# Performance work log

Hardware: AMD Instinct MI355X
Metric: run time of the kernel (lower is better)

Reference implementation:

```python
import jax, jax.numpy as jnp
import numpy as np

INPUT, HIDDEN, LAYERS, OUT = 512, 512, 2, 512
B, T = 128, 1024


def _gru_cell(x, h, w_ih, w_hh, b_ih, b_hh):
    # x: [B, D_in], h: [B, H]; w_ih: [3H, D_in], w_hh: [3H, H]
    gi = x @ w_ih.T + b_ih
    gh = h @ w_hh.T + b_hh
    i_r, i_z, i_n = jnp.split(gi, 3, axis=-1)
    h_r, h_z, h_n = jnp.split(gh, 3, axis=-1)
    r = jax.nn.sigmoid(i_r + h_r)
    z = jax.nn.sigmoid(i_z + h_z)
    n = jnp.tanh(i_n + r * h_n)
    return (1.0 - z) * n + z * h


def setup_inputs() -> dict:
    key = jax.random.key(0)
    ks = jax.random.split(key, 11)
    s = 1.0 / np.sqrt(HIDDEN)
    u = lambda k, shp: jax.random.uniform(k, shp, jnp.float32, -s, s)
    return {
        "x": jax.random.normal(ks[0], (B, T, INPUT), jnp.float32),
        "w_ih0": u(ks[1], (3 * HIDDEN, INPUT)),
        "w_hh0": u(ks[2], (3 * HIDDEN, HIDDEN)),
        "b_ih0": u(ks[3], (3 * HIDDEN,)),
        "b_hh0": u(ks[4], (3 * HIDDEN,)),
        "w_ih1": u(ks[5], (3 * HIDDEN, HIDDEN)),
        "w_hh1": u(ks[6], (3 * HIDDEN, HIDDEN)),
        "b_ih1": u(ks[7], (3 * HIDDEN,)),
        "b_hh1": u(ks[8], (3 * HIDDEN,)),
        "fc_w": u(ks[9], (OUT, HIDDEN)),
        "fc_b": u(ks[10], (OUT,)),
    }


def reference(x, w_ih0, w_hh0, b_ih0, b_hh0, w_ih1, w_hh1, b_ih1, b_hh1, fc_w, fc_b):
    xs = jnp.swapaxes(x, 0, 1)  # [T, B, INPUT]
    h0 = jnp.zeros((x.shape[0], HIDDEN), x.dtype)
    h1 = jnp.zeros((x.shape[0], HIDDEN), x.dtype)

    def step(carry, x_t):
        h0, h1 = carry
        h0 = _gru_cell(x_t, h0, w_ih0, w_hh0, b_ih0, b_hh0)
        h1 = _gru_cell(h0, h1, w_ih1, w_hh1, b_ih1, b_hh1)
        return (h0, h1), None

    (h0, h1), _ = jax.lax.scan(step, (h0, h1), xs)
    # final hidden of top layer -> fc (matches outs[-1].squeeze(); B>1 so squeeze is no-op)
    return h1 @ fc_w.T + fc_b
```

## Files before the change

kernel.cpp:

```cpp
#include <hip/hip_runtime.h>


#define TS   1024
#define HID  512
#define NWG  256
#define WGT  256

typedef __attribute__((ext_vector_type(8))) short bf16x8;
typedef __attribute__((ext_vector_type(4))) unsigned short u16x4;
typedef __attribute__((ext_vector_type(4))) float f32x4;

#define WS_FIN      2048
#define WS_HBUF     8192
#define HBUF_ELEMS  65536
#define WS_H1F      (WS_HBUF + 8 * HBUF_ELEMS * 2)
#define WS_ZERO     (WS_HBUF + 8 * HBUF_ELEMS * 2)

__device__ __forceinline__ unsigned short f2bf(float f) {
    unsigned u = __float_as_uint(f);
    u += 0x7FFFu + ((u >> 16) & 1u);
    return (unsigned short)(u >> 16);
}
__device__ __forceinline__ float bf2f(unsigned short s) {
    return __uint_as_float(((unsigned)s) << 16);
}
__device__ __forceinline__ float sigm(float v) { return 1.0f / (1.0f + __expf(-v)); }
__device__ __forceinline__ float tanh_(float v) { return 1.0f - 2.0f / (1.0f + __expf(2.0f * v)); }

__device__ __forceinline__ void st_agent8(void* p, unsigned long long v) {
    asm volatile("global_store_dwordx2 %0, %1, off sc1" :: "v"(p), "v"(v) : "memory");
}
__device__ __forceinline__ void st_agent16(void* p, f32x4 v) {
    asm volatile("global_store_dwordx4 %0, %1, off sc1" :: "v"(p), "v"(v) : "memory");
}
__device__ __forceinline__ void ld_agent16_issue(bf16x8& d, const unsigned short* p) {
    asm volatile("global_load_dwordx4 %0, %1, off sc1" : "=v"(d) : "v"(p));
}
__device__ __forceinline__ void ld16_issue(f32x4& d, const float* p) {
    asm volatile("global_load_dwordx4 %0, %1, off" : "=v"(d) : "v"(p));
}
__device__ __forceinline__ void wait_vm0() {
    asm volatile("s_waitcnt vmcnt(0)" ::: "memory");
    __builtin_amdgcn_sched_barrier(0);
}
__device__ __forceinline__ f32x4 ld_coh16f(const float* p) {
    const unsigned long long* q = (const unsigned long long*)p;
    union { unsigned long long u[2]; f32x4 v; } r;
    r.u[0] = __hip_atomic_load(q,     __ATOMIC_RELAXED, __HIP_MEMORY_SCOPE_AGENT);
    r.u[1] = __hip_atomic_load(q + 1, __ATOMIC_RELAXED, __HIP_MEMORY_SCOPE_AGENT);
    return r.v;
}

__global__ void __launch_bounds__(WGT, 1)
gru_persistent(const float* __restrict__ x,
               const float* __restrict__ wi0, const float* __restrict__ wh0,
               const float* __restrict__ bi0, const float* __restrict__ bh0,
               const float* __restrict__ wi1, const float* __restrict__ wh1,
               const float* __restrict__ bi1, const float* __restrict__ bh1,
               const float* __restrict__ fcw, const float* __restrict__ fcb,
               float* __restrict__ out, unsigned char* __restrict__ ws)
{
    __shared__ float ldsRed[3][64][49];

    const int tid   = threadIdx.x;
    const int lane  = tid & 63;
    const int kq    = tid >> 6;
    const int wgid  = blockIdx.x;
    const int layer = wgid >> 7;
    const int wid   = wgid & 127;
    const int mtile = wid & 7;
    const int ntile = wid >> 3;
    const int l15   = lane & 15;
    const int l4    = lane >> 4;
    const int gidx  = layer * 16 + ntile;

    unsigned* seqA = (unsigned*)(ws + (size_t)mtile * 256);
    unsigned* fin  = (unsigned*)(ws + WS_FIN);
    unsigned short* hbm = (unsigned short*)(ws + WS_HBUF);
    float* h1f = (float*)(ws + WS_H1F);

    unsigned short* h0hi[2] = { hbm + 0 * HBUF_ELEMS, hbm + 1 * HBUF_ELEMS };
    unsigned short* h0lo[2] = { hbm + 2 * HBUF_ELEMS, hbm + 3 * HBUF_ELEMS };
    unsigned short* h1hi[2] = { hbm + 4 * HBUF_ELEMS, hbm + 5 * HBUF_ELEMS };
    unsigned short* h1lo[2] = { hbm + 6 * HBUF_ELEMS, hbm + 7 * HBUF_ELEMS };

    bf16x8 wiR[4][6], whR[4][6];
    {
        const float* Wi = layer ? wi1 : wi0;
        const float* Wh = layer ? wh1 : wh0;
        #pragma unroll
        for (int kk = 0; kk < 4; ++kk) {
            const int kc = (kq << 2) + kk;
            #pragma unroll
            for (int f = 0; f < 6; ++f) {
                const int g = f >> 1, n2 = f & 1;
                const int jg = g * HID + ntile * 32 + n2 * 16 + l15;
                const float* pi = Wi + (size_t)jg * HID + kc * 32 + (l4 << 3);
                const float* ph = Wh + (size_t)jg * HID + kc * 32 + (l4 << 3);
                #pragma unroll
                for (int e = 0; e < 8; ++e) {
                    wiR[kk][f][e] = (short)f2bf(pi[e]);
                    whR[kk][f][e] = (short)f2bf(ph[e]);
                }
            }
        }
    }

    float br[2][4], bz[2][4], bni[2][4], bnh[2][4];
    if (kq == 0) {
        const float* Bi = layer ? bi1 : bi0;
        const float* Bh = layer ? bh1 : bh0;
        #pragma unroll
        for (int n2 = 0; n2 < 2; ++n2)
            #pragma unroll
            for (int r = 0; r < 4; ++r) {
                int j = ntile * 32 + n2 * 16 + (l4 << 2) + r;
                br[n2][r]  = Bi[j] + Bh[j];
                bz[n2][r]  = Bi[HID + j] + Bh[HID + j];
                bni[n2][r] = Bi[2 * HID + j];
                bnh[n2][r] = Bh[2 * HID + j];
            }
    } else {
        #pragma unroll
        for (int n2 = 0; n2 < 2; ++n2)
            #pragma unroll
            for (int r = 0; r < 4; ++r)
                br[n2][r] = bz[n2][r] = bni[n2][r] = bnh[n2][r] = 0.f;
    }

    float hold[2][4] = {{0,0,0,0},{0,0,0,0}};
    f32x4 acc_i[6], acc_h[6];
    #pragma unroll
    for (int f = 0; f < 6; ++f) {
        acc_i[f] = (f32x4){0.f,0.f,0.f,0.f};
        acc_h[f] = (f32x4){0.f,0.f,0.f,0.f};
    }

    f32x4 xs[4][2];

    auto splitPack = [](float a, float b, unsigned& hiw, unsigned& low) {
        unsigned ba = __float_as_uint(a), bb = __float_as_uint(b);
        unsigned ha = ba & 0xFFFF0000u,   hb = bb & 0xFFFF0000u;
        float la = a - __uint_as_float(ha);
        float lb = b - __uint_as_float(hb);
        hiw = (ba >> 16) | hb;
        low = (__float_as_uint(la) >> 16) | (__float_as_uint(lb) & 0xFFFF0000u);
    };

    auto do_window = [&]() {
        #pragma unroll
        for (int f = 0; f < 6; ++f) acc_i[f] = (f32x4){0.f,0.f,0.f,0.f};
        #pragma unroll
        for (int kk = 0; kk < 4; ++kk) {
            union { unsigned u[4]; bf16x8 v; } hi, lo;
            splitPack(xs[kk][0][0], xs[kk][0][1], hi.u[0], lo.u[0]);
            splitPack(xs[kk][0][2], xs[kk][0][3], hi.u[1], lo.u[1]);
            splitPack(xs[kk][1][0], xs[kk][1][1], hi.u[2], lo.u[2]);
            splitPack(xs[kk][1][2], xs[kk][1][3], hi.u[3], lo.u[3]);
            #pragma unroll
            for (int f = 0; f < 6; ++f) {
                acc_i[f] = __builtin_amdgcn_mfma_f32_16x16x32_bf16(wiR[kk][f], lo.v, acc_i[f], 0, 0, 0);
                acc_i[f] = __builtin_amdgcn_mfma_f32_16x16x32_bf16(wiR[kk][f], hi.v, acc_i[f], 0, 0, 0);
            }
        }
    };

    if (layer == 0) {
        #pragma unroll
        for (int kk = 0; kk < 4; ++kk) {
            const int m = mtile * 16 + l15;
            const int k = ((kq << 2) + kk) * 32 + (l4 << 3);
            const float* xp = x + ((size_t)m * TS + 0) * HID + k;
            ld16_issue(xs[kk][0], xp);
            ld16_issue(xs[kk][1], xp + 4);
        }
        wait_vm0();
        do_window();
    }

    for (int s = 0; s <= TS; ++s) {
        const int wp = s & 1, rp = wp ^ 1;
        const bool active = layer ? (s >= 1) : (s < TS);
        const bool window = (layer == 0) && (s + 1 < TS);
        if (active) {
            #pragma unroll
            for (int f = 0; f < 6; ++f) {
                acc_h[f] = (f32x4){0.f,0.f,0.f,0.f};
                if (layer) acc_i[f] = (f32x4){0.f,0.f,0.f,0.f};
            }

            const unsigned short* pIhi = h0hi[rp];
            const unsigned short* pIlo = h0lo[rp];
            const unsigned short* pHhi = layer ? h1hi[rp] : h0hi[rp];
            const unsigned short* pHlo = layer ? h1lo[rp] : h0lo[rp];

            bf16x8 hH[4][2], hI[4][2];
            #pragma unroll
            for (int kk = 0; kk < 4; ++kk) {
                const int fo = (((mtile * 16 + (kq << 2) + kk) * 64) + lane) * 8;
                ld_agent16_issue(hH[kk][0], pHhi + fo);
                ld_agent16_issue(hH[kk][1], pHlo + fo);
                if (layer) {
                    ld_agent16_issue(hI[kk][0], pIhi + fo);
                    ld_agent16_issue(hI[kk][1], pIlo + fo);
                }
            }
            if (window) {
                #pragma unroll
                for (int kk = 0; kk < 4; ++kk) {
                    const int m = mtile * 16 + l15;
                    const int k = ((kq << 2) + kk) * 32 + (l4 << 3);
                    const float* xp = x + ((size_t)m * TS + (s + 1)) * HID + k;
                    ld16_issue(xs[kk][0], xp);
                    ld16_issue(xs[kk][1], xp + 4);
                }
            }
            wait_vm0();

            #pragma unroll
            for (int kk = 0; kk < 4; ++kk) {
                if (layer) {
                    #pragma unroll
                    for (int f = 0; f < 6; ++f) {
                        acc_i[f] = __builtin_amdgcn_mfma_f32_16x16x32_bf16(wiR[kk][f], hI[kk][1], acc_i[f], 0, 0, 0);
                        acc_i[f] = __builtin_amdgcn_mfma_f32_16x16x32_bf16(wiR[kk][f], hI[kk][0], acc_i[f], 0, 0, 0);
                    }
                }
                #pragma unroll
                for (int f = 0; f < 6; ++f) {
                    acc_h[f] = __builtin_amdgcn_mfma_f32_16x16x32_bf16(whR[kk][f], hH[kk][1], acc_h[f], 0, 0, 0);
                    acc_h[f] = __builtin_amdgcn_mfma_f32_16x16x32_bf16(whR[kk][f], hH[kk][0], acc_h[f], 0, 0, 0);
                }
            }

            if (kq != 0) {
                float* p = &ldsRed[kq - 1][lane][0];
                #pragma unroll
                for (int f = 0; f < 6; ++f) {
                    *(f32x4*)(p + f * 4)      = acc_i[f];
                    *(f32x4*)(p + 24 + f * 4) = acc_h[f];
                }
            }
            __syncthreads();
            if (kq == 0) {
                #pragma unroll
                for (int q = 0; q < 3; ++q) {
                    const float* p = &ldsRed[q][lane][0];
                    #pragma unroll
                    for (int f = 0; f < 6; ++f) {
                        acc_i[f] += *(const f32x4*)(p + f * 4);
                        acc_h[f] += *(const f32x4*)(p + 24 + f * 4);
                    }
                }
                unsigned short* dsthi = layer ? h1hi[wp] : h0hi[wp];
                unsigned short* dstlo = layer ? h1lo[wp] : h0lo[wp];
                #pragma unroll
                for (int n2 = 0; n2 < 2; ++n2) {
                    u16x4 shi, slo; f32x4 hv;
                    #pragma unroll
                    for (int r = 0; r < 4; ++r) {
                        float vr = acc_i[n2][r]     + acc_h[n2][r]     + br[n2][r];
                        float vz = acc_i[2 + n2][r] + acc_h[2 + n2][r] + bz[n2][r];
                        float rg = sigm(vr);
                        float zg = sigm(vz);
                        float ng = tanh_(acc_i[4 + n2][r] + bni[n2][r] + rg * (acc_h[4 + n2][r] + bnh[n2][r]));
                        float h  = (1.0f - zg) * ng + zg * hold[n2][r];
                        hold[n2][r] = h;
                        hv[r] = h;
                        unsigned short hb = f2bf(h);
                        shi[r] = hb;
                        slo[r] = f2bf(h - bf2f(hb));
                    }
                    const int eo = (((mtile * 16 + ntile) * 64) + l15 + (n2 * 2 + (l4 >> 1)) * 16) * 8
                                 + (l4 & 1) * 4;
                    st_agent8(dsthi + eo, __builtin_bit_cast(unsigned long long, shi));
                    st_agent8(dstlo + eo, __builtin_bit_cast(unsigned long long, slo));
                    if (layer && s == TS) {
                        const int m = mtile * 16 + l15;
                        st_agent16(h1f + (size_t)m * HID + ntile * 32 + n2 * 16 + (l4 << 2), hv);
                    }
                }
            }
        }

        if (tid == 0) {
            asm volatile("s_waitcnt vmcnt(0)" ::: "memory");
            __hip_atomic_store(&seqA[gidx], (unsigned)(s + 1),
                               __ATOMIC_RELAXED, __HIP_MEMORY_SCOPE_AGENT);
        }

        if (window) do_window();

        if (kq == 0) {
            const unsigned tgt = (unsigned)(s + 1);
            const unsigned long long* sp =
                (const unsigned long long*)(seqA + ((lane & 7) << 2));
            const int paddr = lane << 9;
            for (;;) {
                unsigned probe;
                asm volatile("ds_read_b32 %0, %1\n\ts_waitcnt lgkmcnt(0)"
                             : "=v"(probe) : "v"(paddr));
                bool ok = true;
                if (lane < 8) {
                    unsigned long long a = __hip_atomic_load(sp,     __ATOMIC_RELAXED, __HIP_MEMORY_SCOPE_AGENT);
                    unsigned long long b = __hip_atomic_load(sp + 1, __ATOMIC_RELAXED, __HIP_MEMORY_SCOPE_AGENT);
                    ok = ((unsigned)a >= tgt) && ((unsigned)(a >> 32) >= tgt) &&
                         ((unsigned)b >= tgt) && ((unsigned)(b >> 32) >= tgt);
                }
                if (__all(ok)) break;
                __builtin_amdgcn_s_sleep(1);
            }
        }
        __syncthreads();
    }

    if (tid == 0) {
        asm volatile("s_waitcnt vmcnt(0)" ::: "memory");
        __hip_atomic_fetch_add(fin, 1u, __ATOMIC_RELAXED, __HIP_MEMORY_SCOPE_AGENT);
    }
    if (wgid < 64) {
        float* fw = &ldsRed[0][0][0];
        const float* src = fcw + (size_t)wgid * 8 * HID;
        for (int i = tid; i < (8 * HID) / 4; i += WGT) {
            f32x4 v = *(const f32x4*)(src + i * 4);
            int row = (i * 4) >> 9;
            int kk  = (i * 4) & 511;
            *(f32x4*)(fw + row * 516 + kk) = v;
        }
        if (tid == 0) {
            while (__hip_atomic_load(fin, __ATOMIC_RELAXED, __HIP_MEMORY_SCOPE_AGENT) < (unsigned)NWG)
                __builtin_amdgcn_s_sleep(1);
        }
        __syncthreads();
        const int col = wgid * 8 + (tid & 7);
        const int m0  = tid >> 3;
        float a0 = fcb[col], a1 = a0, a2 = a0, a3 = a0;
        const float* fwr = fw + (tid & 7) * 516;
        for (int k = 0; k < HID; k += 4) {
            f32x4 wv  = *(const f32x4*)(fwr + k);
            f32x4 h0v = ld_coh16f(h1f + (size_t)(m0)      * HID + k);
            f32x4 h1v = ld_coh16f(h1f + (size_t)(m0 + 32) * HID + k);
            f32x4 h2v = ld_coh16f(h1f + (size_t)(m0 + 64) * HID + k);
            f32x4 h3v = ld_coh16f(h1f + (size_t)(m0 + 96) * HID + k);
            a0 += h0v[0]*wv[0] + h0v[1]*wv[1] + h0v[2]*wv[2] + h0v[3]*wv[3];
            a1 += h1v[0]*wv[0] + h1v[1]*wv[1] + h1v[2]*wv[2] + h1v[3]*wv[3];
            a2 += h2v[0]*wv[0] + h2v[1]*wv[1] + h2v[2]*wv[2] + h2v[3]*wv[3];
            a3 += h3v[0]*wv[0] + h3v[1]*wv[1] + h3v[2]*wv[2] + h3v[3]*wv[3];
        }
        out[(size_t)(m0)      * HID + col] = a0;
        out[(size_t)(m0 + 32) * HID + col] = a1;
        out[(size_t)(m0 + 64) * HID + col] = a2;
        out[(size_t)(m0 + 96) * HID + col] = a3;
    }
}

extern "C" void kernel_launch(void* const* d_in, const int* in_sizes, int n_in,
                              void* d_out, int out_size, void* d_ws, size_t ws_size,
                              hipStream_t stream) {
    (void)in_sizes; (void)n_in; (void)out_size; (void)ws_size;
    hipMemsetAsync(d_ws, 0, WS_ZERO, stream);
    gru_persistent<<<dim3(NWG), dim3(WGT), 0, stream>>>(
        (const float*)d_in[0],
        (const float*)d_in[1], (const float*)d_in[2],
        (const float*)d_in[3], (const float*)d_in[4],
        (const float*)d_in[5], (const float*)d_in[6],
        (const float*)d_in[7], (const float*)d_in[8],
        (const float*)d_in[9], (const float*)d_in[10],
        (float*)d_out, (unsigned char*)d_ws);
}
```

Before: 8.824 ms.

## Double workgroup count, halving per-WG hidden tile to 16 columns

Splits the recurrent GEMM across 512 persistent workgroups instead of 256, so each workgroup owns 16 hidden columns (3 gate fragments) instead of 32. Launch bounds allow two workgroups per CU, and the LDS reduction buffer, register weights and accumulators are halved. The goal is to shorten the serial per-step MFMA chain on the critical path. In exchange, each step's barrier must poll twice as many sequence counters, and the h-buffer store layout changes to match the finer tiling.

```diff
diff --git a/kernel.cpp b/kernel.cpp
--- a/kernel.cpp
+++ b/kernel.cpp
@@ -3,14 +3,14 @@
 
 #define TS   1024
 #define HID  512
-#define NWG  256
+#define NWG  512
 #define WGT  256
 
 typedef __attribute__((ext_vector_type(8))) short bf16x8;
 typedef __attribute__((ext_vector_type(4))) unsigned short u16x4;
 typedef __attribute__((ext_vector_type(4))) float f32x4;
 
-#define WS_FIN      2048
+#define WS_FIN      4096
 #define WS_HBUF     8192
 #define HBUF_ELEMS  65536
 #define WS_H1F      (WS_HBUF + 8 * HBUF_ELEMS * 2)
@@ -50,8 +50,16 @@
     r.u[1] = __hip_atomic_load(q + 1, __ATOMIC_RELAXED, __HIP_MEMORY_SCOPE_AGENT);
     return r.v;
 }
-
-__global__ void __launch_bounds__(WGT, 1)
+__device__ __forceinline__ void splitPack2(float a, float b, unsigned& hiw, unsigned& low) {
+    unsigned ba = __float_as_uint(a), bb = __float_as_uint(b);
+    unsigned ha = ba & 0xFFFF0000u,   hb = bb & 0xFFFF0000u;
+    float la = a - __uint_as_float(ha);
+    float lb = b - __uint_as_float(hb);
+    hiw = (ba >> 16) | hb;
+    low = (__float_as_uint(la) >> 16) | (__float_as_uint(lb) & 0xFFFF0000u);
+}
+
+__global__ void __launch_bounds__(WGT, 2)
 gru_persistent(const float* __restrict__ x,
                const float* __restrict__ wi0, const float* __restrict__ wh0,
                const float* __restrict__ bi0, const float* __restrict__ bh0,
@@ -60,21 +68,21 @@
                const float* __restrict__ fcw, const float* __restrict__ fcb,
                float* __restrict__ out, unsigned char* __restrict__ ws)
 {
-    __shared__ float ldsRed[3][64][49];
+    __shared__ float ldsRed[3][64][25];
 
     const int tid   = threadIdx.x;
     const int lane  = tid & 63;
     const int kq    = tid >> 6;
     const int wgid  = blockIdx.x;
-    const int layer = wgid >> 7;
-    const int wid   = wgid & 127;
-    const int mtile = wid & 7;
-    const int ntile = wid >> 3;
+    const int layer = wgid >> 8;
+    const int wid   = wgid & 255;
+    const int mt    = wid & 7;
+    const int nt    = wid >> 3;
     const int l15   = lane & 15;
     const int l4    = lane >> 4;
-    const int gidx  = layer * 16 + ntile;
-
-    unsigned* seqA = (unsigned*)(ws + (size_t)mtile * 256);
+    const int gidx  = layer * 32 + nt;
+
+    unsigned* seqA = (unsigned*)(ws + (size_t)mt * 256);
     unsigned* fin  = (unsigned*)(ws + WS_FIN);
     unsigned short* hbm = (unsigned short*)(ws + WS_HBUF);
     float* h1f = (float*)(ws + WS_H1F);
@@ -84,7 +92,7 @@
     unsigned short* h1hi[2] = { hbm + 4 * HBUF_ELEMS, hbm + 5 * HBUF_ELEMS };
     unsigned short* h1lo[2] = { hbm + 6 * HBUF_ELEMS, hbm + 7 * HBUF_ELEMS };
 
-    bf16x8 wiR[4][6], whR[4][6];
+    bf16x8 wiR[4][3], whR[4][3];
     {
         const float* Wi = layer ? wi1 : wi0;
         const float* Wh = layer ? wh1 : wh0;
@@ -92,75 +100,60 @@
         for (int kk = 0; kk < 4; ++kk) {
             const int kc = (kq << 2) + kk;
             #pragma unroll
-            for (int f = 0; f < 6; ++f) {
-                const int g = f >> 1, n2 = f & 1;
-                const int jg = g * HID + ntile * 32 + n2 * 16 + l15;
+            for (int g = 0; g < 3; ++g) {
+                const int jg = g * HID + nt * 16 + l15;
                 const float* pi = Wi + (size_t)jg * HID + kc * 32 + (l4 << 3);
                 const float* ph = Wh + (size_t)jg * HID + kc * 32 + (l4 << 3);
                 #pragma unroll
                 for (int e = 0; e < 8; ++e) {
-                    wiR[kk][f][e] = (short)f2bf(pi[e]);
-                    whR[kk][f][e] = (short)f2bf(ph[e]);
-                }
-            }
-        }
-    }
-
-    float br[2][4], bz[2][4], bni[2][4], bnh[2][4];
+                    wiR[kk][g][e] = (short)f2bf(pi[e]);
+                    whR[kk][g][e] = (short)f2bf(ph[e]);
+                }
+            }
+        }
+    }
+
+    float br[4], bz[4], bni[4], bnh[4];
     if (kq == 0) {
         const float* Bi = layer ? bi1 : bi0;
         const float* Bh = layer ? bh1 : bh0;
         #pragma unroll
-        for (int n2 = 0; n2 < 2; ++n2)
-            #pragma unroll
-            for (int r = 0; r < 4; ++r) {
-                int j = ntile * 32 + n2 * 16 + (l4 << 2) + r;
-                br[n2][r]  = Bi[j] + Bh[j];
-                bz[n2][r]  = Bi[HID + j] + Bh[HID + j];
-                bni[n2][r] = Bi[2 * HID + j];
-                bnh[n2][r] = Bh[2 * HID + j];
-            }
+        for (int r = 0; r < 4; ++r) {
+            int j = nt * 16 + (l4 << 2) + r;
+            br[r]  = Bi[j] + Bh[j];
+            bz[r]  = Bi[HID + j] + Bh[HID + j];
+            bni[r] = Bi[2 * HID + j];
+            bnh[r] = Bh[2 * HID + j];
+        }
     } else {
         #pragma unroll
-        for (int n2 = 0; n2 < 2; ++n2)
-            #pragma unroll
-            for (int r = 0; r < 4; ++r)
-                br[n2][r] = bz[n2][r] = bni[n2][r] = bnh[n2][r] = 0.f;
-    }
-
-    float hold[2][4] = {{0,0,0,0},{0,0,0,0}};
-    f32x4 acc_i[6], acc_h[6];
+        for (int r = 0; r < 4; ++r) br[r] = bz[r] = bni[r] = bnh[r] = 0.f;
+    }
+
+    float hold[4] = {0,0,0,0};
+    f32x4 acc_i[3], acc_h[3];
     #pragma unroll
-    for (int f = 0; f < 6; ++f) {
-        acc_i[f] = (f32x4){0.f,0.f,0.f,0.f};
-        acc_h[f] = (f32x4){0.f,0.f,0.f,0.f};
+    for (int g = 0; g < 3; ++g) {
+        acc_i[g] = (f32x4){0.f,0.f,0.f,0.f};
+        acc_h[g] = (f32x4){0.f,0.f,0.f,0.f};
     }
 
     f32x4 xs[4][2];
 
-    auto splitPack = [](float a, float b, unsigned& hiw, unsigned& low) {
-        unsigned ba = __float_as_uint(a), bb = __float_as_uint(b);
-        unsigned ha = ba & 0xFFFF0000u,   hb = bb & 0xFFFF0000u;
-        float la = a - __uint_as_float(ha);
-        float lb = b - __uint_as_float(hb);
-        hiw = (ba >> 16) | hb;
-        low = (__float_as_uint(la) >> 16) | (__float_as_uint(lb) & 0xFFFF0000u);
-    };
-
     auto do_window = [&]() {
         #pragma unroll
-        for (int f = 0; f < 6; ++f) acc_i[f] = (f32x4){0.f,0.f,0.f,0.f};
+        for (int g = 0; g < 3; ++g) acc_i[g] = (f32x4){0.f,0.f,0.f,0.f};
         #pragma unroll
         for (int kk = 0; kk < 4; ++kk) {
             union { unsigned u[4]; bf16x8 v; } hi, lo;
-            splitPack(xs[kk][0][0], xs[kk][0][1], hi.u[0], lo.u[0]);
-            splitPack(xs[kk][0][2], xs[kk][0][3], hi.u[1], lo.u[1]);
-            splitPack(xs[kk][1][0], xs[kk][1][1], hi.u[2], lo.u[2]);
-            splitPack(xs[kk][1][2], xs[kk][1][3], hi.u[3], lo.u[3]);
-            #pragma unroll
-            for (int f = 0; f < 6; ++f) {
-                acc_i[f] = __builtin_amdgcn_mfma_f32_16x16x32_bf16(wiR[kk][f], lo.v, acc_i[f], 0, 0, 0);
-                acc_i[f] = __builtin_amdgcn_mfma_f32_16x16x32_bf16(wiR[kk][f], hi.v, acc_i[f], 0, 0, 0);
+            splitPack2(xs[kk][0][0], xs[kk][0][1], hi.u[0], lo.u[0]);
+            splitPack2(xs[kk][0][2], xs[kk][0][3], hi.u[1], lo.u[1]);
+            splitPack2(xs[kk][1][0], xs[kk][1][1], hi.u[2], lo.u[2]);
+            splitPack2(xs[kk][1][2], xs[kk][1][3], hi.u[3], lo.u[3]);
+            #pragma unroll
+            for (int g = 0; g < 3; ++g) {
+                acc_i[g] = __builtin_amdgcn_mfma_f32_16x16x32_bf16(wiR[kk][g], lo.v, acc_i[g], 0, 0, 0);
+                acc_i[g] = __builtin_amdgcn_mfma_f32_16x16x32_bf16(wiR[kk][g], hi.v, acc_i[g], 0, 0, 0);
             }
         }
     };
@@ -168,7 +161,7 @@
     if (layer == 0) {
         #pragma unroll
         for (int kk = 0; kk < 4; ++kk) {
-            const int m = mtile * 16 + l15;
+            const int m = mt * 16 + l15;
             const int k = ((kq << 2) + kk) * 32 + (l4 << 3);
             const float* xp = x + ((size_t)m * TS + 0) * HID + k;
             ld16_issue(xs[kk][0], xp);
@@ -184,9 +177,9 @@
         const bool window = (layer == 0) && (s + 1 < TS);
         if (active) {
             #pragma unroll
-            for (int f = 0; f < 6; ++f) {
-                acc_h[f] = (f32x4){0.f,0.f,0.f,0.f};
-                if (layer) acc_i[f] = (f32x4){0.f,0.f,0.f,0.f};
+            for (int g = 0; g < 3; ++g) {
+                acc_h[g] = (f32x4){0.f,0.f,0.f,0.f};
+                if (layer) acc_i[g] = (f32x4){0.f,0.f,0.f,0.f};
             }
 
             const unsigned short* pIhi = h0hi[rp];
@@ -197,7 +190,7 @@
             bf16x8 hH[4][2], hI[4][2];
             #pragma unroll
             for (int kk = 0; kk < 4; ++kk) {
-                const int fo = (((mtile * 16 + (kq << 2) + kk) * 64) + lane) * 8;
+                const int fo = (((mt * 16 + (kq << 2) + kk) * 64) + lane) * 8;
                 ld_agent16_issue(hH[kk][0], pHhi + fo);
                 ld_agent16_issue(hH[kk][1], pHlo + fo);
                 if (layer) {
@@ -208,7 +201,7 @@
             if (window) {
                 #pragma unroll
                 for (int kk = 0; kk < 4; ++kk) {
-                    const int m = mtile * 16 + l15;
+                    const int m = mt * 16 + l15;
                     const int k = ((kq << 2) + kk) * 32 + (l4 << 3);
                     const float* xp = x + ((size_t)m * TS + (s + 1)) * HID + k;
                     ld16_issue(xs[kk][0], xp);
@@ -221,24 +214,24 @@
             for (int kk = 0; kk < 4; ++kk) {
                 if (layer) {
                     #pragma unroll
-                    for (int f = 0; f < 6; ++f) {
-                        acc_i[f] = __builtin_amdgcn_mfma_f32_16x16x32_bf16(wiR[kk][f], hI[kk][1], acc_i[f], 0, 0, 0);
-                        acc_i[f] = __builtin_amdgcn_mfma_f32_16x16x32_bf16(wiR[kk][f], hI[kk][0], acc_i[f], 0, 0, 0);
+                    for (int g = 0; g < 3; ++g) {
+                        acc_i[g] = __builtin_amdgcn_mfma_f32_16x16x32_bf16(wiR[kk][g], hI[kk][1], acc_i[g], 0, 0, 0);
+                        acc_i[g] = __builtin_amdgcn_mfma_f32_16x16x32_bf16(wiR[kk][g], hI[kk][0], acc_i[g], 0, 0, 0);
                     }
                 }
                 #pragma unroll
-                for (int f = 0; f < 6; ++f) {
-                    acc_h[f] = __builtin_amdgcn_mfma_f32_16x16x32_bf16(whR[kk][f], hH[kk][1], acc_h[f], 0, 0, 0);
-                    acc_h[f] = __builtin_amdgcn_mfma_f32_16x16x32_bf16(whR[kk][f], hH[kk][0], acc_h[f], 0, 0, 0);
+                for (int g = 0; g < 3; ++g) {
+                    acc_h[g] = __builtin_amdgcn_mfma_f32_16x16x32_bf16(whR[kk][g], hH[kk][1], acc_h[g], 0, 0, 0);
+                    acc_h[g] = __builtin_amdgcn_mfma_f32_16x16x32_bf16(whR[kk][g], hH[kk][0], acc_h[g], 0, 0, 0);
                 }
             }
 
             if (kq != 0) {
                 float* p = &ldsRed[kq - 1][lane][0];
                 #pragma unroll
-                for (int f = 0; f < 6; ++f) {
-                    *(f32x4*)(p + f * 4)      = acc_i[f];
-                    *(f32x4*)(p + 24 + f * 4) = acc_h[f];
+                for (int g = 0; g < 3; ++g) {
+                    *(f32x4*)(p + g * 4)      = acc_i[g];
+                    *(f32x4*)(p + 12 + g * 4) = acc_h[g];
                 }
             }
             __syncthreads();
@@ -247,38 +240,34 @@
                 for (int q = 0; q < 3; ++q) {
                     const float* p = &ldsRed[q][lane][0];
                     #pragma unroll
-                    for (int f = 0; f < 6; ++f) {
-                        acc_i[f] += *(const f32x4*)(p + f * 4);
-                        acc_h[f] += *(const f32x4*)(p + 24 + f * 4);
+                    for (int g = 0; g < 3; ++g) {
+                        acc_i[g] += *(const f32x4*)(p + g * 4);
+                        acc_h[g] += *(const f32x4*)(p + 12 + g * 4);
                     }
                 }
                 unsigned short* dsthi = layer ? h1hi[wp] : h0hi[wp];
                 unsigned short* dstlo = layer ? h1lo[wp] : h0lo[wp];
-                #pragma unroll
-                for (int n2 = 0; n2 < 2; ++n2) {
-                    u16x4 shi, slo; f32x4 hv;
-                    #pragma unroll
-                    for (int r = 0; r < 4; ++r) {
-                        float vr = acc_i[n2][r]     + acc_h[n2][r]     + br[n2][r];
-                        float vz = acc_i[2 + n2][r] + acc_h[2 + n2][r] + bz[n2][r];
-                        float rg = sigm(vr);
-                        float zg = sigm(vz);
-                        float ng = tanh_(acc_i[4 + n2][r] + bni[n2][r] + rg * (acc_h[4 + n2][r] + bnh[n2][r]));
-                        float h  = (1.0f - zg) * ng + zg * hold[n2][r];
-                        hold[n2][r] = h;
-                        hv[r] = h;
-                        unsigned short hb = f2bf(h);
-                        shi[r] = hb;
-                        slo[r] = f2bf(h - bf2f(hb));
-                    }
-                    const int eo = (((mtile * 16 + ntile) * 64) + l15 + (n2 * 2 + (l4 >> 1)) * 16) * 8
-                                 + (l4 & 1) * 4;
-                    st_agent8(dsthi + eo, __builtin_bit_cast(unsigned long long, shi));
-                    st_agent8(dstlo + eo, __builtin_bit_cast(unsigned long long, slo));
-                    if (layer && s == TS) {
-                        const int m = mtile * 16 + l15;
-                        st_agent16(h1f + (size_t)m * HID + ntile * 32 + n2 * 16 + (l4 << 2), hv);
-                    }
+                u16x4 shi, slo; f32x4 hv;
+                #pragma unroll
+                for (int r = 0; r < 4; ++r) {
+                    float vr = acc_i[0][r] + acc_h[0][r] + br[r];
+                    float vz = acc_i[1][r] + acc_h[1][r] + bz[r];
+                    float rg = sigm(vr);
+                    float zg = sigm(vz);
+                    float ng = tanh_(acc_i[2][r] + bni[r] + rg * (acc_h[2][r] + bnh[r]));
+                    float h  = (1.0f - zg) * ng + zg * hold[r];
+                    hold[r] = h; hv[r] = h;
+                    unsigned short hb = f2bf(h);
+                    shi[r] = hb;
+                    slo[r] = f2bf(h - bf2f(hb));
+                }
+                const int lanep = l15 + ((((nt & 1) << 1) + (l4 >> 1)) << 4);
+                const int eo = (((mt * 16 + (nt >> 1)) * 64) + lanep) * 8 + (l4 & 1) * 4;
+                st_agent8(dsthi + eo, __builtin_bit_cast(unsigned long long, shi));
+                st_agent8(dstlo + eo, __builtin_bit_cast(unsigned long long, slo));
+                if (layer && s == TS) {
+                    const int m = mt * 16 + l15;
+                    st_agent16(h1f + (size_t)m * HID + nt * 16 + (l4 << 2), hv);
                 }
             }
         }
@@ -293,15 +282,15 @@
 
         if (kq == 0) {
             const unsigned tgt = (unsigned)(s + 1);
-            const unsigned long long* sp =
-                (const unsigned long long*)(seqA + ((lane & 7) << 2));
-            const int paddr = lane << 9;
+            const int paddr = lane << 8;
             for (;;) {
                 unsigned probe;
                 asm volatile("ds_read_b32 %0, %1\n\ts_waitcnt lgkmcnt(0)"
                              : "=v"(probe) : "v"(paddr));
                 bool ok = true;
-                if (lane < 8) {
+                if (lane < 16) {
+                    const unsigned long long* sp =
+                        (const unsigned long long*)(seqA + (lane << 2));
                     unsigned long long a = __hip_atomic_load(sp,     __ATOMIC_RELAXED, __HIP_MEMORY_SCOPE_AGENT);
                     unsigned long long b = __hip_atomic_load(sp + 1, __ATOMIC_RELAXED, __HIP_MEMORY_SCOPE_AGENT);
                     ok = ((unsigned)a >= tgt) && ((unsigned)(a >> 32) >= tgt) &&
```

Result: slower. 11.53 ms (+30.7%).
